# Kernel optimization log

Measured on AMD Instinct MI355X. Metric: run time of the kernel, lower is better.

## Reference

```python
import jax, jax.numpy as jnp
import numpy as np

D_IN = 1024
D_OUT = 1024
NUM_HEADS = 16
HEAD_DIM = D_OUT // NUM_HEADS


def setup_inputs() -> dict:
    key = jax.random.key(0)
    k = jax.random.split(key, 6)
    s = 1.0 / np.sqrt(D_IN)
    return {
        "x": jax.random.normal(k[0], (2, 2048, D_IN), dtype=jnp.float32),
        "W_q": jax.random.uniform(k[1], (D_OUT, D_IN), jnp.float32, -s, s),
        "W_k": jax.random.uniform(k[2], (D_OUT, D_IN), jnp.float32, -s, s),
        "W_v": jax.random.uniform(k[3], (D_OUT, D_IN), jnp.float32, -s, s),
        "W_o": jax.random.uniform(k[4], (D_OUT, D_OUT), jnp.float32, -s, s),
        "b_o": jax.random.uniform(k[5], (D_OUT,), jnp.float32, -s, s),
    }


def reference(x, W_q, W_k, W_v, W_o, b_o):
    b, n, _ = x.shape
    h, hd = NUM_HEADS, HEAD_DIM
    # linear projections (torch Linear: x @ W.T), reshape to [b, h, n, hd]
    q = (x @ W_q.T).reshape(b, n, h, hd).transpose(0, 2, 1, 3)
    k = (x @ W_k.T).reshape(b, n, h, hd).transpose(0, 2, 1, 3)
    v = (x @ W_v.T).reshape(b, n, h, hd).transpose(0, 2, 1, 3)
    scores = jnp.einsum("bhqd,bhkd->bhqk", q, k) / np.sqrt(hd).astype(np.float32)
    causal = jnp.triu(jnp.full((n, n), -jnp.inf, dtype=scores.dtype), k=1)
    scores = scores + causal[None, None]
    weights = jax.nn.softmax(scores, axis=-1)  # dropout p=0.0 -> identity
    ctx = jnp.einsum("bhqk,bhkd->bhqd", weights, v)
    ctx = ctx.transpose(0, 2, 1, 3).reshape(b, n, h * hd)
    return ctx @ W_o.T + b_o
```

## Files before the change

### kernel.cpp

```cpp
#include <hip/hip_runtime.h>
#include <hip/hip_bf16.h>
#include <stdint.h>

typedef __attribute__((ext_vector_type(8)))  __bf16   bf16x8;
typedef __attribute__((ext_vector_type(4)))  float    f32x4;
typedef __attribute__((ext_vector_type(16))) float    f32x16;
typedef __attribute__((ext_vector_type(4)))  unsigned u32x4;
typedef __attribute__((ext_vector_type(2)))  unsigned u32x2;

#define BATCH  2
#define SEQ    2048
#define DMODEL 1024
#define NHEAD  16
#define HDIM   64
#define MTOT   (BATCH * SEQ)
#define MOFF   8.0f

__device__ __forceinline__ void gload_lds16(const void* g, void* l) {
  __builtin_amdgcn_global_load_lds(
      (const __attribute__((address_space(1))) unsigned int*)g,
      (__attribute__((address_space(3))) unsigned int*)(uintptr_t)l,
      16, 0, 0);
}

__device__ __forceinline__ unsigned pkbf(float a, float b) {
  unsigned lo = (unsigned)__builtin_bit_cast(unsigned short, (__bf16)a);
  unsigned hb = (unsigned)__builtin_bit_cast(unsigned short, (__bf16)b);
  return lo | (hb << 16);
}

__global__ void cast_all(const float* __restrict__ x,  const float* __restrict__ wq,
                         const float* __restrict__ wk, const float* __restrict__ wv,
                         const float* __restrict__ wo,
                         __bf16* __restrict__ xb,  __bf16* __restrict__ wqb,
                         __bf16* __restrict__ wkb, __bf16* __restrict__ wvb,
                         __bf16* __restrict__ wob)
{
  const float* in; __bf16* out; int n;
  switch (blockIdx.y) {
    case 0:  in = x;  out = xb;  n = MTOT * DMODEL;   break;
    case 1:  in = wq; out = wqb; n = DMODEL * DMODEL; break;
    case 2:  in = wk; out = wkb; n = DMODEL * DMODEL; break;
    case 3:  in = wv; out = wvb; n = DMODEL * DMODEL; break;
    default: in = wo; out = wob; n = DMODEL * DMODEL; break;
  }
  const int i = blockIdx.x * blockDim.x + threadIdx.x;
  const int stride = gridDim.x * blockDim.x;
  for (int idx = i; idx * 8 < n; idx += stride) {
    const float4 a = ((const float4*)in)[idx * 2];
    const float4 b = ((const float4*)in)[idx * 2 + 1];
    bf16x8 v = { (__bf16)a.x, (__bf16)a.y, (__bf16)a.z, (__bf16)a.w,
                 (__bf16)b.x, (__bf16)b.y, (__bf16)b.z, (__bf16)b.w };
    *(bf16x8*)(out + (size_t)idx * 8) = v;
  }
}

__device__ __forceinline__ void gemm_tile_128(const __bf16* __restrict__ A,
                                              const __bf16* __restrict__ W,
                                              int bm, int bn, int Kd,
                                              f32x4 (&acc)[4][4])
{
  __shared__ __align__(16) __bf16 As[128 * 32];
  __shared__ __align__(16) __bf16 Bs[128 * 32];
  const int tid  = threadIdx.x;
  const int wave = tid >> 6, lane = tid & 63;
  const int wr = wave >> 1, wc = wave & 1;
  const int fr = lane & 15, fq = lane >> 4;
  const int c0 = tid, c1 = tid + 256;
  const __bf16* gA0 = A + (size_t)(bm * 128 + (c0 >> 2)) * Kd + (c0 & 3) * 8;
  const __bf16* gA1 = A + (size_t)(bm * 128 + (c1 >> 2)) * Kd + (c1 & 3) * 8;
  const __bf16* gB0 = W + (size_t)(bn * 128 + (c0 >> 2)) * Kd + (c0 & 3) * 8;
  const __bf16* gB1 = W + (size_t)(bn * 128 + (c1 >> 2)) * Kd + (c1 & 3) * 8;

  for (int k0 = 0; k0 < Kd; k0 += 32) {
    gload_lds16(gA0 + k0, As + c0 * 8);
    gload_lds16(gB0 + k0, Bs + c0 * 8);
    gload_lds16(gA1 + k0, As + c1 * 8);
    gload_lds16(gB1 + k0, Bs + c1 * 8);
    __syncthreads();
    bf16x8 a[4], b[4];
#pragma unroll
    for (int m = 0; m < 4; ++m)
      a[m] = *(const bf16x8*)(As + (wr * 64 + m * 16 + fr) * 32 + fq * 8);
#pragma unroll
    for (int n = 0; n < 4; ++n)
      b[n] = *(const bf16x8*)(Bs + (wc * 64 + n * 16 + fr) * 32 + fq * 8);
#pragma unroll
    for (int m = 0; m < 4; ++m)
#pragma unroll
      for (int n = 0; n < 4; ++n)
        acc[m][n] = __builtin_amdgcn_mfma_f32_16x16x32_bf16(a[m], b[n], acc[m][n], 0, 0, 0);
    __syncthreads();
  }
}

__global__ __launch_bounds__(256)
void gemm_qkv(const __bf16* __restrict__ xb,
              const __bf16* __restrict__ Wq, const __bf16* __restrict__ Wk,
              const __bf16* __restrict__ Wv,
              __bf16* __restrict__ Qo, __bf16* __restrict__ Ko, __bf16* __restrict__ VTo,
              float qscale)
{
  const int z = blockIdx.z;
  const __bf16* A; const __bf16* W; __bf16* Ob; float scale; int bm, bn, Nn;
  if (z == 2)      { A = Wv; W = xb; Ob = VTo; scale = 1.f;    bm = blockIdx.y; bn = blockIdx.x; Nn = MTOT;   }
  else if (z == 1) { A = xb; W = Wk; Ob = Ko;  scale = 1.f;    bm = blockIdx.x; bn = blockIdx.y; Nn = DMODEL; }
  else             { A = xb; W = Wq; Ob = Qo;  scale = qscale; bm = blockIdx.x; bn = blockIdx.y; Nn = DMODEL; }

  f32x4 acc[4][4] = {};
  gemm_tile_128(A, W, bm, bn, DMODEL, acc);

  const int lane = threadIdx.x & 63, wave = threadIdx.x >> 6;
  const int wr = wave >> 1, wc = wave & 1;
  const int fr = lane & 15, fq = lane >> 4;
#pragma unroll
  for (int m = 0; m < 4; ++m)
#pragma unroll
    for (int n = 0; n < 4; ++n) {
      const int col = bn * 128 + wc * 64 + n * 16 + fr;
#pragma unroll
      for (int j = 0; j < 4; ++j) {
        const int row = bm * 128 + wr * 64 + m * 16 + fq * 4 + j;
        Ob[(size_t)row * Nn + col] = (__bf16)(acc[m][n][j] * scale);
      }
    }
}

__global__ __launch_bounds__(256)
void gemm_out(const __bf16* __restrict__ A, const __bf16* __restrict__ W,
              float* __restrict__ OF, const float* __restrict__ bias)
{
  f32x4 acc[4][4] = {};
  gemm_tile_128(A, W, blockIdx.x, blockIdx.y, DMODEL, acc);

  const int lane = threadIdx.x & 63, wave = threadIdx.x >> 6;
  const int wr = wave >> 1, wc = wave & 1;
  const int fr = lane & 15, fq = lane >> 4;
#pragma unroll
  for (int m = 0; m < 4; ++m)
#pragma unroll
    for (int n = 0; n < 4; ++n) {
      const int col = blockIdx.y * 128 + wc * 64 + n * 16 + fr;
#pragma unroll
      for (int j = 0; j < 4; ++j) {
        const int row = blockIdx.x * 128 + wr * 64 + m * 16 + fq * 4 + j;
        OF[(size_t)row * DMODEL + col] = acc[m][n][j] + bias[col];
      }
    }
}


__device__ __forceinline__ void mask_tile(f32x16& sv0, f32x16& sv1,
                                          int kv0, int q0, int ln, int hi)
{
  const int qg = q0 + ln;
#pragma unroll
  for (int r = 0; r < 16; ++r) {
    const int kvo = kv0 + (r & 3) + 8 * (r >> 2) + 4 * hi;
    if (kvo > qg)      sv0[r] = -1e30f;
    if (kvo + 32 > qg) sv1[r] = -1e30f;
  }
}

__device__ __forceinline__ void stream_fin(f32x16& sv0, f32x16& sv1, float& l_acc,
                                           f32x16& c0, f32x16& c1,
                                           const bf16x8 (&vt0)[4], const bf16x8 (&vt1)[4],
                                           int hi)
{
#pragma unroll
  for (int r = 0; r < 16; ++r) {
    sv0[r] = __builtin_amdgcn_exp2f(sv0[r] - MOFF);
    sv1[r] = __builtin_amdgcn_exp2f(sv1[r] - MOFF);
  }
  float s8[8];
#pragma unroll
  for (int r = 0; r < 8; ++r)
    s8[r] = (sv0[r] + sv0[r + 8]) + (sv1[r] + sv1[r + 8]);
#pragma unroll
  for (int r = 0; r < 4; ++r) s8[r] += s8[r + 4];
  l_acc += (s8[0] + s8[1]) + (s8[2] + s8[3]);

  bf16x8 pf[4];
#pragma unroll
  for (int half = 0; half < 2; ++half) {
    const int r0 = half * 8;
    {
      unsigned pk01 = pkbf(sv0[r0 + 0], sv0[r0 + 1]);
      unsigned pk23 = pkbf(sv0[r0 + 2], sv0[r0 + 3]);
      unsigned pk45 = pkbf(sv0[r0 + 4], sv0[r0 + 5]);
      unsigned pk67 = pkbf(sv0[r0 + 6], sv0[r0 + 7]);
      unsigned x01 = (unsigned)__shfl_xor((int)pk01, 32, 64);
      unsigned x23 = (unsigned)__shfl_xor((int)pk23, 32, 64);
      unsigned x45 = (unsigned)__shfl_xor((int)pk45, 32, 64);
      unsigned x67 = (unsigned)__shfl_xor((int)pk67, 32, 64);
      u32x4 uw = { hi ? x45 : pk01, hi ? x67 : pk23,
                   hi ? pk45 : x01, hi ? pk67 : x23 };
      pf[half] = __builtin_bit_cast(bf16x8, uw);
    }
    {
      unsigned pk01 = pkbf(sv1[r0 + 0], sv1[r0 + 1]);
      unsigned pk23 = pkbf(sv1[r0 + 2], sv1[r0 + 3]);
      unsigned pk45 = pkbf(sv1[r0 + 4], sv1[r0 + 5]);
      unsigned pk67 = pkbf(sv1[r0 + 6], sv1[r0 + 7]);
      unsigned x01 = (unsigned)__shfl_xor((int)pk01, 32, 64);
      unsigned x23 = (unsigned)__shfl_xor((int)pk23, 32, 64);
      unsigned x45 = (unsigned)__shfl_xor((int)pk45, 32, 64);
      unsigned x67 = (unsigned)__shfl_xor((int)pk67, 32, 64);
      u32x4 uw = { hi ? x45 : pk01, hi ? x67 : pk23,
                   hi ? pk45 : x01, hi ? pk67 : x23 };
      pf[2 + half] = __builtin_bit_cast(bf16x8, uw);
    }
  }

  __builtin_amdgcn_s_setprio(1);
#pragma unroll
  for (int kc = 0; kc < 4; ++kc)
    c0 = __builtin_amdgcn_mfma_f32_32x32x16_bf16(vt0[kc], pf[kc], c0, 0, 0, 0);
#pragma unroll
  for (int kc = 0; kc < 4; ++kc)
    c1 = __builtin_amdgcn_mfma_f32_32x32x16_bf16(vt1[kc], pf[kc], c1, 0, 0, 0);
  __builtin_amdgcn_s_setprio(0);
}

__global__ __launch_bounds__(128, 2)
void attn_kernel(const __bf16* __restrict__ Qg, const __bf16* __restrict__ Kg,
                 const __bf16* __restrict__ VTg, __bf16* __restrict__ Og)
{
  __shared__ __align__(16) float Cs[2][32][68];
  __shared__ float Ls[2][2][32];

  const int tid  = threadIdx.x;
  const int p    = tid >> 6;
  const int lane = tid & 63;
  const int ln = lane & 31, hi = lane >> 5;
  const int bI = blockIdx.x;
  const int bh = bI & 31;
  const int jp = bI >> 5;
  const int b = bh >> 4, h = bh & 15;

  const int qtL = jp, qtH = 63 - jp;
  const int q0L = qtL * 32, q0H = qtH * 32;
  const int ntL = (qtL >> 1) + 1, ntH = (qtH >> 1) + 1;

  const __bf16* Kp  = Kg  + (size_t)b * SEQ * DMODEL + h * HDIM + hi * 8;
  const __bf16* Vp  = VTg + (size_t)(h * HDIM) * MTOT + (size_t)b * SEQ + hi * 8;
  const __bf16* QpL = Qg + ((size_t)b * SEQ + q0L + ln) * DMODEL + h * HDIM + hi * 8;
  const __bf16* QpH = Qg + ((size_t)b * SEQ + q0H + ln) * DMODEL + h * HDIM + hi * 8;

  bf16x8 qfL[4], qfH[4];
#pragma unroll
  for (int kc = 0; kc < 4; ++kc) {
    qfL[kc] = *(const bf16x8*)(QpL + kc * 16);
    qfH[kc] = *(const bf16x8*)(QpH + kc * 16);
  }

  f32x16 cL0 = {}, cL1 = {}, cH0 = {}, cH1 = {};
  float lL = 0.f, lH = 0.f;

  for (int t = p; t < ntH; t += 2) {
    const int kv0 = t * 64;

    bf16x8 kA[4], kB[4], vt0[4], vt1[4];
#pragma unroll
    for (int kc = 0; kc < 4; ++kc) {
      kA[kc]  = *(const bf16x8*)(Kp + (size_t)(kv0 + ln) * DMODEL + kc * 16);
      kB[kc]  = *(const bf16x8*)(Kp + (size_t)(kv0 + 32 + ln) * DMODEL + kc * 16);
      vt0[kc] = *(const bf16x8*)(Vp + (size_t)ln * MTOT + kv0 + kc * 16);
      vt1[kc] = *(const bf16x8*)(Vp + (size_t)(32 + ln) * MTOT + kv0 + kc * 16);
    }

    {
      f32x16 s0 = {}, s1 = {};
      __builtin_amdgcn_s_setprio(1);
#pragma unroll
      for (int kc = 0; kc < 4; ++kc) {
        s0 = __builtin_amdgcn_mfma_f32_32x32x16_bf16(kA[kc], qfH[kc], s0, 0, 0, 0);
        s1 = __builtin_amdgcn_mfma_f32_32x32x16_bf16(kB[kc], qfH[kc], s1, 0, 0, 0);
      }
      __builtin_amdgcn_s_setprio(0);
      if (t == ntH - 1) mask_tile(s0, s1, kv0, q0H, ln, hi);
      stream_fin(s0, s1, lH, cH0, cH1, vt0, vt1, hi);
    }

    if (t < ntL) {
      f32x16 s0 = {}, s1 = {};
      __builtin_amdgcn_s_setprio(1);
#pragma unroll
      for (int kc = 0; kc < 4; ++kc) {
        s0 = __builtin_amdgcn_mfma_f32_32x32x16_bf16(kA[kc], qfL[kc], s0, 0, 0, 0);
        s1 = __builtin_amdgcn_mfma_f32_32x32x16_bf16(kB[kc], qfL[kc], s1, 0, 0, 0);
      }
      __builtin_amdgcn_s_setprio(0);
      if (t == ntL - 1) mask_tile(s0, s1, kv0, q0L, ln, hi);
      stream_fin(s0, s1, lL, cL0, cL1, vt0, vt1, hi);
    }
  }

  if (p == 0) {
#pragma unroll
    for (int g = 0; g < 4; ++g) {
      f32x4 v0 = { cH0[4*g+0], cH0[4*g+1], cH0[4*g+2], cH0[4*g+3] };
      f32x4 v1 = { cH1[4*g+0], cH1[4*g+1], cH1[4*g+2], cH1[4*g+3] };
      *(f32x4*)&Cs[1][ln][g * 8 + hi * 4]      = v0;
      *(f32x4*)&Cs[1][ln][32 + g * 8 + hi * 4] = v1;
    }
    Ls[1][hi][ln] = lH;
  } else {
#pragma unroll
    for (int g = 0; g < 4; ++g) {
      f32x4 v0 = { cL0[4*g+0], cL0[4*g+1], cL0[4*g+2], cL0[4*g+3] };
      f32x4 v1 = { cL1[4*g+0], cL1[4*g+1], cL1[4*g+2], cL1[4*g+3] };
      *(f32x4*)&Cs[0][ln][g * 8 + hi * 4]      = v0;
      *(f32x4*)&Cs[0][ln][32 + g * 8 + hi * 4] = v1;
    }
    Ls[0][hi][ln] = lL;
  }
  __syncthreads();

  if (p == 0) {
    const float lt = lL + __shfl_xor(lL, 32, 64) + Ls[0][0][ln] + Ls[0][1][ln];
    const float inv = 1.0f / lt;
    __bf16* Op = Og + ((size_t)b * SEQ + q0L + ln) * DMODEL + h * HDIM;
#pragma unroll
    for (int g = 0; g < 4; ++g) {
      const f32x4 u0 = *(const f32x4*)&Cs[0][ln][g * 8 + hi * 4];
      const f32x4 u1 = *(const f32x4*)&Cs[0][ln][32 + g * 8 + hi * 4];
      u32x2 w;
      w.x = pkbf((cL0[4*g+0] + u0[0]) * inv, (cL0[4*g+1] + u0[1]) * inv);
      w.y = pkbf((cL0[4*g+2] + u0[2]) * inv, (cL0[4*g+3] + u0[3]) * inv);
      *(u32x2*)(Op + g * 8 + hi * 4) = w;
      w.x = pkbf((cL1[4*g+0] + u1[0]) * inv, (cL1[4*g+1] + u1[1]) * inv);
      w.y = pkbf((cL1[4*g+2] + u1[2]) * inv, (cL1[4*g+3] + u1[3]) * inv);
      *(u32x2*)(Op + 32 + g * 8 + hi * 4) = w;
    }
  } else {
    const float lt = lH + __shfl_xor(lH, 32, 64) + Ls[1][0][ln] + Ls[1][1][ln];
    const float inv = 1.0f / lt;
    __bf16* Op = Og + ((size_t)b * SEQ + q0H + ln) * DMODEL + h * HDIM;
#pragma unroll
    for (int g = 0; g < 4; ++g) {
      const f32x4 u0 = *(const f32x4*)&Cs[1][ln][g * 8 + hi * 4];
      const f32x4 u1 = *(const f32x4*)&Cs[1][ln][32 + g * 8 + hi * 4];
      u32x2 w;
      w.x = pkbf((cH0[4*g+0] + u0[0]) * inv, (cH0[4*g+1] + u0[1]) * inv);
      w.y = pkbf((cH0[4*g+2] + u0[2]) * inv, (cH0[4*g+3] + u0[3]) * inv);
      *(u32x2*)(Op + g * 8 + hi * 4) = w;
      w.x = pkbf((cH1[4*g+0] + u1[0]) * inv, (cH1[4*g+1] + u1[1]) * inv);
      w.y = pkbf((cH1[4*g+2] + u1[2]) * inv, (cH1[4*g+3] + u1[3]) * inv);
      *(u32x2*)(Op + 32 + g * 8 + hi * 4) = w;
    }
  }
}

extern "C" void kernel_launch(void* const* d_in, const int* in_sizes, int n_in,
                              void* d_out, int out_size, void* d_ws, size_t ws_size,
                              hipStream_t stream) {
  (void)in_sizes; (void)n_in; (void)out_size; (void)ws_size;
  const float* x  = (const float*)d_in[0];
  const float* Wq = (const float*)d_in[1];
  const float* Wk = (const float*)d_in[2];
  const float* Wv = (const float*)d_in[3];
  const float* Wo = (const float*)d_in[4];
  const float* bo = (const float*)d_in[5];
  float* out = (float*)d_out;

  __bf16* ws  = (__bf16*)d_ws;
  __bf16* xb  = ws;
  __bf16* Wqb = xb  + (size_t)MTOT * DMODEL;
  __bf16* Wkb = Wqb + (size_t)DMODEL * DMODEL;
  __bf16* Wvb = Wkb + (size_t)DMODEL * DMODEL;
  __bf16* Wob = Wvb + (size_t)DMODEL * DMODEL;
  __bf16* Qb  = Wob + (size_t)DMODEL * DMODEL;
  __bf16* Kb  = Qb  + (size_t)MTOT * DMODEL;
  __bf16* VTb = Kb  + (size_t)MTOT * DMODEL;
  __bf16* ctxb = xb;

  cast_all<<<dim3(256, 5), 256, 0, stream>>>(x, Wq, Wk, Wv, Wo,
                                             xb, Wqb, Wkb, Wvb, Wob);

  const float qscale = 0.125f * 1.4426950408889634f;
  gemm_qkv<<<dim3(32, 8, 3), 256, 0, stream>>>(xb, Wqb, Wkb, Wvb, Qb, Kb, VTb, qscale);

  attn_kernel<<<dim3(1024), 128, 0, stream>>>(Qb, Kb, VTb, ctxb);

  gemm_out<<<dim3(32, 8), 256, 0, stream>>>(ctxb, Wob, out, bo);
}
```

Baseline: 121.0 us.

## Split attention KV loop across four waves with shared-memory reduction epilogue

Attention blocks grow from two to four wavefronts, each handling every fourth KV tile for both the low and high query tiles. The epilogue becomes a four-way reduction through shared memory, done in two phases (low tile, then high tile), with each thread writing 16-byte output chunks. The K and V loads are also split into separate loops. This shortens the serial KV loop per wave and adds parallelism on long causal rows, at the cost of more shared memory, extra barriers, and higher register pressure from the 256-thread, 4-blocks-per-CU launch bound.

```diff
diff --git a/kernel.cpp b/kernel.cpp
--- a/kernel.cpp
+++ b/kernel.cpp
@@ -222,12 +222,12 @@
   __builtin_amdgcn_s_setprio(0);
 }
 
-__global__ __launch_bounds__(128, 2)
+__global__ __launch_bounds__(256, 4)
 void attn_kernel(const __bf16* __restrict__ Qg, const __bf16* __restrict__ Kg,
                  const __bf16* __restrict__ VTg, __bf16* __restrict__ Og)
 {
-  __shared__ __align__(16) float Cs[2][32][68];
-  __shared__ float Ls[2][2][32];
+  __shared__ __align__(16) float Cs[4][32][68];
+  __shared__ float Ls[4][2][32];
 
   const int tid  = threadIdx.x;
   const int p    = tid >> 6;
@@ -257,7 +257,7 @@
   f32x16 cL0 = {}, cL1 = {}, cH0 = {}, cH1 = {};
   float lL = 0.f, lH = 0.f;
 
-  for (int t = p; t < ntH; t += 2) {
+  for (int t = p; t < ntH; t += 4) {
     const int kv0 = t * 64;
 
     bf16x8 kA[4], kB[4], vt0[4], vt1[4];
@@ -265,6 +265,9 @@
     for (int kc = 0; kc < 4; ++kc) {
       kA[kc]  = *(const bf16x8*)(Kp + (size_t)(kv0 + ln) * DMODEL + kc * 16);
       kB[kc]  = *(const bf16x8*)(Kp + (size_t)(kv0 + 32 + ln) * DMODEL + kc * 16);
+    }
+#pragma unroll
+    for (int kc = 0; kc < 4; ++kc) {
       vt0[kc] = *(const bf16x8*)(Vp + (size_t)ln * MTOT + kv0 + kc * 16);
       vt1[kc] = *(const bf16x8*)(Vp + (size_t)(32 + ln) * MTOT + kv0 + kc * 16);
     }
@@ -296,59 +299,60 @@
     }
   }
 
-  if (p == 0) {
-#pragma unroll
-    for (int g = 0; g < 4; ++g) {
-      f32x4 v0 = { cH0[4*g+0], cH0[4*g+1], cH0[4*g+2], cH0[4*g+3] };
-      f32x4 v1 = { cH1[4*g+0], cH1[4*g+1], cH1[4*g+2], cH1[4*g+3] };
-      *(f32x4*)&Cs[1][ln][g * 8 + hi * 4]      = v0;
-      *(f32x4*)&Cs[1][ln][32 + g * 8 + hi * 4] = v1;
-    }
-    Ls[1][hi][ln] = lH;
-  } else {
-#pragma unroll
-    for (int g = 0; g < 4; ++g) {
-      f32x4 v0 = { cL0[4*g+0], cL0[4*g+1], cL0[4*g+2], cL0[4*g+3] };
-      f32x4 v1 = { cL1[4*g+0], cL1[4*g+1], cL1[4*g+2], cL1[4*g+3] };
-      *(f32x4*)&Cs[0][ln][g * 8 + hi * 4]      = v0;
-      *(f32x4*)&Cs[0][ln][32 + g * 8 + hi * 4] = v1;
-    }
-    Ls[0][hi][ln] = lL;
-  }
+  const int qe = (p << 3) | (lane >> 3);
+  const int de = (lane & 7) * 8;
+
+#pragma unroll
+  for (int g = 0; g < 4; ++g) {
+    f32x4 v0 = { cL0[4*g+0], cL0[4*g+1], cL0[4*g+2], cL0[4*g+3] };
+    f32x4 v1 = { cL1[4*g+0], cL1[4*g+1], cL1[4*g+2], cL1[4*g+3] };
+    *(f32x4*)&Cs[p][ln][g * 8 + hi * 4]      = v0;
+    *(f32x4*)&Cs[p][ln][32 + g * 8 + hi * 4] = v1;
+  }
+  Ls[p][hi][ln] = lL;
   __syncthreads();
 
-  if (p == 0) {
-    const float lt = lL + __shfl_xor(lL, 32, 64) + Ls[0][0][ln] + Ls[0][1][ln];
+  {
+    float lt = 0.f;
+#pragma unroll
+    for (int pp = 0; pp < 4; ++pp) lt += Ls[pp][0][qe] + Ls[pp][1][qe];
     const float inv = 1.0f / lt;
-    __bf16* Op = Og + ((size_t)b * SEQ + q0L + ln) * DMODEL + h * HDIM;
-#pragma unroll
-    for (int g = 0; g < 4; ++g) {
-      const f32x4 u0 = *(const f32x4*)&Cs[0][ln][g * 8 + hi * 4];
-      const f32x4 u1 = *(const f32x4*)&Cs[0][ln][32 + g * 8 + hi * 4];
-      u32x2 w;
-      w.x = pkbf((cL0[4*g+0] + u0[0]) * inv, (cL0[4*g+1] + u0[1]) * inv);
-      w.y = pkbf((cL0[4*g+2] + u0[2]) * inv, (cL0[4*g+3] + u0[3]) * inv);
-      *(u32x2*)(Op + g * 8 + hi * 4) = w;
-      w.x = pkbf((cL1[4*g+0] + u1[0]) * inv, (cL1[4*g+1] + u1[1]) * inv);
-      w.y = pkbf((cL1[4*g+2] + u1[2]) * inv, (cL1[4*g+3] + u1[3]) * inv);
-      *(u32x2*)(Op + 32 + g * 8 + hi * 4) = w;
-    }
-  } else {
-    const float lt = lH + __shfl_xor(lH, 32, 64) + Ls[1][0][ln] + Ls[1][1][ln];
+    f32x4 a0 = {}, a1 = {};
+#pragma unroll
+    for (int pp = 0; pp < 4; ++pp) {
+      a0 += *(const f32x4*)&Cs[pp][qe][de];
+      a1 += *(const f32x4*)&Cs[pp][qe][de + 4];
+    }
+    u32x4 w = { pkbf(a0[0] * inv, a0[1] * inv), pkbf(a0[2] * inv, a0[3] * inv),
+                pkbf(a1[0] * inv, a1[1] * inv), pkbf(a1[2] * inv, a1[3] * inv) };
+    *(u32x4*)(Og + ((size_t)b * SEQ + q0L + qe) * DMODEL + h * HDIM + de) = w;
+  }
+  __syncthreads();
+
+#pragma unroll
+  for (int g = 0; g < 4; ++g) {
+    f32x4 v0 = { cH0[4*g+0], cH0[4*g+1], cH0[4*g+2], cH0[4*g+3] };
+    f32x4 v1 = { cH1[4*g+0], cH1[4*g+1], cH1[4*g+2], cH1[4*g+3] };
+    *(f32x4*)&Cs[p][ln][g * 8 + hi * 4]      = v0;
+    *(f32x4*)&Cs[p][ln][32 + g * 8 + hi * 4] = v1;
+  }
+  Ls[p][hi][ln] = lH;
+  __syncthreads();
+
+  {
+    float lt = 0.f;
+#pragma unroll
+    for (int pp = 0; pp < 4; ++pp) lt += Ls[pp][0][qe] + Ls[pp][1][qe];
     const float inv = 1.0f / lt;
-    __bf16* Op = Og + ((size_t)b * SEQ + q0H + ln) * DMODEL + h * HDIM;
-#pragma unroll
-    for (int g = 0; g < 4; ++g) {
-      const f32x4 u0 = *(const f32x4*)&Cs[1][ln][g * 8 + hi * 4];
-      const f32x4 u1 = *(const f32x4*)&Cs[1][ln][32 + g * 8 + hi * 4];
-      u32x2 w;
-      w.x = pkbf((cH0[4*g+0] + u0[0]) * inv, (cH0[4*g+1] + u0[1]) * inv);
-      w.y = pkbf((cH0[4*g+2] + u0[2]) * inv, (cH0[4*g+3] + u0[3]) * inv);
-      *(u32x2*)(Op + g * 8 + hi * 4) = w;
-      w.x = pkbf((cH1[4*g+0] + u1[0]) * inv, (cH1[4*g+1] + u1[1]) * inv);
-      w.y = pkbf((cH1[4*g+2] + u1[2]) * inv, (cH1[4*g+3] + u1[3]) * inv);
-      *(u32x2*)(Op + 32 + g * 8 + hi * 4) = w;
-    }
+    f32x4 a0 = {}, a1 = {};
+#pragma unroll
+    for (int pp = 0; pp < 4; ++pp) {
+      a0 += *(const f32x4*)&Cs[pp][qe][de];
+      a1 += *(const f32x4*)&Cs[pp][qe][de + 4];
+    }
+    u32x4 w = { pkbf(a0[0] * inv, a0[1] * inv), pkbf(a0[2] * inv, a0[3] * inv),
+                pkbf(a1[0] * inv, a1[1] * inv), pkbf(a1[2] * inv, a1[3] * inv) };
+    *(u32x4*)(Og + ((size_t)b * SEQ + q0H + qe) * DMODEL + h * HDIM + de) = w;
   }
 }
 
@@ -381,7 +385,7 @@
   const float qscale = 0.125f * 1.4426950408889634f;
   gemm_qkv<<<dim3(32, 8, 3), 256, 0, stream>>>(xb, Wqb, Wkb, Wvb, Qb, Kb, VTb, qscale);
 
-  attn_kernel<<<dim3(1024), 128, 0, stream>>>(Qb, Kb, VTb, ctxb);
+  attn_kernel<<<dim3(1024), 256, 0, stream>>>(Qb, Kb, VTb, ctxb);
 
   gemm_out<<<dim3(32, 8), 256, 0, stream>>>(ctxb, Wob, out, bo);
 }
```

Measured after the change: 273.6 us. +126.1%, slower.

## Pre-pack K and V into MFMA fragment order for coalesced attention loads

Applied to the files above, without the earlier changes.

The QKV GEMM epilogue now writes K and V^T straight into a per-head, per-tile packed layout that matches the register fragments the attention MFMAs consume. Each attention tile load then becomes a contiguous 16-byte-per-lane read instead of strided rows across DMODEL or MTOT. The aim is to cut scattered global traffic in the attention inner loop. In exchange the GEMM epilogue does scattered 2-byte stores with more index arithmetic.

```diff
diff --git a/kernel.cpp b/kernel.cpp
--- a/kernel.cpp
+++ b/kernel.cpp
@@ -102,10 +102,10 @@
               float qscale)
 {
   const int z = blockIdx.z;
-  const __bf16* A; const __bf16* W; __bf16* Ob; float scale; int bm, bn, Nn;
-  if (z == 2)      { A = Wv; W = xb; Ob = VTo; scale = 1.f;    bm = blockIdx.y; bn = blockIdx.x; Nn = MTOT;   }
-  else if (z == 1) { A = xb; W = Wk; Ob = Ko;  scale = 1.f;    bm = blockIdx.x; bn = blockIdx.y; Nn = DMODEL; }
-  else             { A = xb; W = Wq; Ob = Qo;  scale = qscale; bm = blockIdx.x; bn = blockIdx.y; Nn = DMODEL; }
+  const __bf16* A; const __bf16* W; __bf16* Ob; int bm, bn;
+  if (z == 2)      { A = Wv; W = xb; Ob = VTo; bm = blockIdx.y; bn = blockIdx.x; }
+  else if (z == 1) { A = xb; W = Wk; Ob = Ko;  bm = blockIdx.x; bn = blockIdx.y; }
+  else             { A = xb; W = Wq; Ob = Qo;  bm = blockIdx.x; bn = blockIdx.y; }
 
   f32x4 acc[4][4] = {};
   gemm_tile_128(A, W, bm, bn, DMODEL, acc);
@@ -113,17 +113,57 @@
   const int lane = threadIdx.x & 63, wave = threadIdx.x >> 6;
   const int wr = wave >> 1, wc = wave & 1;
   const int fr = lane & 15, fq = lane >> 4;
-#pragma unroll
-  for (int m = 0; m < 4; ++m)
-#pragma unroll
-    for (int n = 0; n < 4; ++n) {
-      const int col = bn * 128 + wc * 64 + n * 16 + fr;
-#pragma unroll
-      for (int j = 0; j < 4; ++j) {
-        const int row = bm * 128 + wr * 64 + m * 16 + fq * 4 + j;
-        Ob[(size_t)row * Nn + col] = (__bf16)(acc[m][n][j] * scale);
-      }
-    }
+
+  if (z == 0) {
+#pragma unroll
+    for (int m = 0; m < 4; ++m)
+#pragma unroll
+      for (int n = 0; n < 4; ++n) {
+        const int col = bn * 128 + wc * 64 + n * 16 + fr;
+#pragma unroll
+        for (int j = 0; j < 4; ++j) {
+          const int row = bm * 128 + wr * 64 + m * 16 + fq * 4 + j;
+          Ob[(size_t)row * DMODEL + col] = (__bf16)(acc[m][n][j] * qscale);
+        }
+      }
+  } else if (z == 1) {
+#pragma unroll
+    for (int m = 0; m < 4; ++m)
+#pragma unroll
+      for (int n = 0; n < 4; ++n) {
+        const int f = bn * 128 + wc * 64 + n * 16 + fr;
+        const int h = f >> 6;
+        const int kc = (f >> 4) & 3, hi = (f >> 3) & 1, jj = f & 7;
+#pragma unroll
+        for (int j = 0; j < 4; ++j) {
+          const int tkn = bm * 128 + wr * 64 + m * 16 + fq * 4 + j;
+          const int bb = tkn >> 11, n2 = tkn & 2047;
+          const int t32 = n2 >> 5, ln2 = n2 & 31;
+          const size_t idx = (((((size_t)bb * 16 + h) * 64 + t32) * 4 + kc) * 64
+                              + (ln2 + (hi << 5))) * 8 + jj;
+          Ob[idx] = (__bf16)acc[m][n][j];
+        }
+      }
+  } else {
+#pragma unroll
+    for (int m = 0; m < 4; ++m)
+#pragma unroll
+      for (int n = 0; n < 4; ++n) {
+        const int tkn = bn * 128 + wc * 64 + n * 16 + fr;
+        const int bb = tkn >> 11, n2 = tkn & 2047;
+        const int t64 = n2 >> 6, w2 = n2 & 63;
+        const int kc = w2 >> 4, hi = (w2 >> 3) & 1, jj = w2 & 7;
+#pragma unroll
+        for (int j = 0; j < 4; ++j) {
+          const int f = bm * 128 + wr * 64 + m * 16 + fq * 4 + j;
+          const int h = f >> 6, d = f & 63;
+          const int db = d >> 5, ln2 = d & 31;
+          const size_t idx = ((((((size_t)bb * 16 + h) * 32 + t64) * 2 + db) * 4 + kc) * 64
+                              + (ln2 + (hi << 5))) * 8 + jj;
+          Ob[idx] = (__bf16)acc[m][n][j];
+        }
+      }
+  }
 }
 
 __global__ __launch_bounds__(256)
@@ -223,8 +263,8 @@
 }
 
 __global__ __launch_bounds__(128, 2)
-void attn_kernel(const __bf16* __restrict__ Qg, const __bf16* __restrict__ Kg,
-                 const __bf16* __restrict__ VTg, __bf16* __restrict__ Og)
+void attn_kernel(const __bf16* __restrict__ Qg, const __bf16* __restrict__ PK,
+                 const __bf16* __restrict__ PV, __bf16* __restrict__ Og)
 {
   __shared__ __align__(16) float Cs[2][32][68];
   __shared__ float Ls[2][2][32];
@@ -242,8 +282,8 @@
   const int q0L = qtL * 32, q0H = qtH * 32;
   const int ntL = (qtL >> 1) + 1, ntH = (qtH >> 1) + 1;
 
-  const __bf16* Kp  = Kg  + (size_t)b * SEQ * DMODEL + h * HDIM + hi * 8;
-  const __bf16* Vp  = VTg + (size_t)(h * HDIM) * MTOT + (size_t)b * SEQ + hi * 8;
+  const __bf16* Kp  = PK + (size_t)(b * 16 + h) * (64 * 4 * 64 * 8);
+  const __bf16* Vp  = PV + (size_t)(b * 16 + h) * (32 * 2 * 4 * 64 * 8);
   const __bf16* QpL = Qg + ((size_t)b * SEQ + q0L + ln) * DMODEL + h * HDIM + hi * 8;
   const __bf16* QpH = Qg + ((size_t)b * SEQ + q0H + ln) * DMODEL + h * HDIM + hi * 8;
 
@@ -258,16 +298,22 @@
   float lL = 0.f, lH = 0.f;
 
   for (int t = p; t < ntH; t += 2) {
+    const __bf16* kt = Kp + (size_t)t * 4096;
+    const __bf16* vt = Vp + (size_t)t * 4096;
+
+    bf16x8 kA[4], kB[4], vt0[4], vt1[4];
+#pragma unroll
+    for (int kc = 0; kc < 4; ++kc) {
+      kA[kc]  = *(const bf16x8*)(kt + (kc * 64 + lane) * 8);
+      kB[kc]  = *(const bf16x8*)(kt + 2048 + (kc * 64 + lane) * 8);
+    }
+#pragma unroll
+    for (int kc = 0; kc < 4; ++kc) {
+      vt0[kc] = *(const bf16x8*)(vt + (kc * 64 + lane) * 8);
+      vt1[kc] = *(const bf16x8*)(vt + 2048 + (kc * 64 + lane) * 8);
+    }
+
     const int kv0 = t * 64;
-
-    bf16x8 kA[4], kB[4], vt0[4], vt1[4];
-#pragma unroll
-    for (int kc = 0; kc < 4; ++kc) {
-      kA[kc]  = *(const bf16x8*)(Kp + (size_t)(kv0 + ln) * DMODEL + kc * 16);
-      kB[kc]  = *(const bf16x8*)(Kp + (size_t)(kv0 + 32 + ln) * DMODEL + kc * 16);
-      vt0[kc] = *(const bf16x8*)(Vp + (size_t)ln * MTOT + kv0 + kc * 16);
-      vt1[kc] = *(const bf16x8*)(Vp + (size_t)(32 + ln) * MTOT + kv0 + kc * 16);
-    }
 
     {
       f32x16 s0 = {}, s1 = {};
@@ -371,17 +417,17 @@
   __bf16* Wvb = Wkb + (size_t)DMODEL * DMODEL;
   __bf16* Wob = Wvb + (size_t)DMODEL * DMODEL;
   __bf16* Qb  = Wob + (size_t)DMODEL * DMODEL;
-  __bf16* Kb  = Qb  + (size_t)MTOT * DMODEL;
-  __bf16* VTb = Kb  + (size_t)MTOT * DMODEL;
+  __bf16* Kpk = Qb  + (size_t)MTOT * DMODEL;
+  __bf16* Vpk = Kpk + (size_t)MTOT * DMODEL;
   __bf16* ctxb = xb;
 
   cast_all<<<dim3(256, 5), 256, 0, stream>>>(x, Wq, Wk, Wv, Wo,
                                              xb, Wqb, Wkb, Wvb, Wob);
 
   const float qscale = 0.125f * 1.4426950408889634f;
-  gemm_qkv<<<dim3(32, 8, 3), 256, 0, stream>>>(xb, Wqb, Wkb, Wvb, Qb, Kb, VTb, qscale);
-
-  attn_kernel<<<dim3(1024), 128, 0, stream>>>(Qb, Kb, VTb, ctxb);
+  gemm_qkv<<<dim3(32, 8, 3), 256, 0, stream>>>(xb, Wqb, Wkb, Wvb, Qb, Kpk, Vpk, qscale);
+
+  attn_kernel<<<dim3(1024), 128, 0, stream>>>(Qb, Kpk, Vpk, ctxb);
 
   gemm_out<<<dim3(32, 8), 256, 0, stream>>>(ctxb, Wob, out, bo);
 }
```

After: 100.1 us. 1.21x faster.
